# Kernel tuning notes

Measured on AMD Instinct MI355X. Metric: run time of the kernel, lower is better.

## Reference

```python
import jax, jax.numpy as jnp
import numpy as np

DIM = 1024
NB = 25            # num_basis_functions
ALPHA_X = 1.0
DT = 0.001
MAX_TIME = 10.0
TAU = 1.0
ALPHA_Y = 25.0
BETA_Y = 6.25
WEIGHT_SCALE = 1000.0
T = int(MAX_TIME / DT) + 1   # rollout buffer length = 10001


def setup_inputs() -> dict:
    key = jax.random.key(0)
    k1, k2, k3 = jax.random.split(key, 3)
    y0 = jax.random.normal(k1, (DIM,), dtype=jnp.float32)
    # learned parameters of the module
    g = jax.random.normal(k2, (DIM,), dtype=jnp.float32)
    weights = jax.random.normal(k3, (DIM, NB), dtype=jnp.float32) / NB
    return {"y0": y0, "g": g, "weights": weights}


def reference(y0, g, weights):
    # basis function centers / widths (canonical system)
    c = jnp.exp(-ALPHA_X * jnp.linspace(0.0, MAX_TIME, NB)).astype(y0.dtype)
    h = (NB / c).astype(y0.dtype)
    decay = jnp.asarray(1.0 - ALPHA_X * TAU * DT, y0.dtype)

    def step(carry, _):
        x, y, dy = carry
        x = x * decay                                   # decay_time()
        psi = jnp.exp(-h * (x - c) ** 2)                # [NB]
        # force(y0): sum over basis functions, per dim
        force = (WEIGHT_SCALE * (weights @ psi)) * x * (g - y0) / jnp.sum(psi)  # [DIM]
        ddy = ALPHA_Y * (BETA_Y * (g - y) - dy) + force
        ndy = dy + TAU * DT * ddy
        ny = y + TAU * DT * ndy
        return (x, ny, ndy), jnp.concatenate([ny, ndy])

    x0 = jnp.asarray(1.0, y0.dtype)
    dy0 = jnp.zeros_like(y0)
    _, rows = jax.lax.scan(step, (x0, y0, dy0), None, length=T - 1)  # [T-1, 2*DIM]
    first = jnp.concatenate([y0, dy0])[None]                          # [1, 2*DIM]
    ydy = jnp.concatenate([first, rows], axis=0)                      # [T, 2*DIM]
    y0rep = jnp.broadcast_to(y0, (T, DIM))
    return jnp.concatenate([y0rep, ydy], axis=1)                      # [T, 3*DIM]
```

## Files before the change

### kernel.cpp

```cpp
#include <hip/hip_runtime.h>
#include <math.h>


#define DIM    1024
#define NB     25
#define NSTEP  10000
#define CHUNKS 200
#define LSTEPS 50
#define QS     32

__global__ __launch_bounds__(64) void k_prep(float* __restrict__ q,
                                             float* __restrict__ QY,
                                             float* __restrict__ QD,
                                             double logdecay,
                                             double a00, double a01,
                                             double a10, double a11) {
    __shared__ float lq[LSTEPS][NB + 1];
    const int c = blockIdx.x;
    const int tid = threadIdx.x;
    if (tid < LSTEPS) {
        int t = c * LSTEPS + tid + 1;
        float x = (float)exp((double)t * logdecay);
        float psi[NB];
        float S = 0.f;
#pragma unroll
        for (int k = 0; k < NB; ++k) {
            float lk = (10.0f / 24.0f) * (float)k;
            float ck = expf(-lk);
            float hk = 25.0f / ck;
            float dxc = x - ck;
            float p = expf(-hk * dxc * dxc);
            psi[k] = p;
            S += p;
        }
        float scale = 1000.0f * x / S;
        float* qrow = q + (size_t)(c * LSTEPS + tid) * QS;
#pragma unroll
        for (int k = 0; k < NB; ++k) {
            float v = psi[k] * scale;
            qrow[k] = v;
            lq[tid][k] = v;
        }
    }
    __syncthreads();
    if (tid < NB) {
        double py = (double)0.001f * (double)0.001f;
        double pd = (double)0.001f;
        double qy = 0.0, qd = 0.0;
        for (int j = LSTEPS - 1; j >= 0; --j) {
            double v = (double)lq[j][tid];
            qy += py * v;
            qd += pd * v;
            double npy = a00 * py + a01 * pd;
            double npd = a10 * py + a11 * pd;
            py = npy; pd = npd;
        }
        QY[c * QS + tid] = (float)qy;
        QD[c * QS + tid] = (float)qd;
    }
}

__global__ __launch_bounds__(256) void k_dots(const float* __restrict__ QY,
                                              const float* __restrict__ QD,
                                              const float* __restrict__ W,
                                              const float* __restrict__ g,
                                              const float* __restrict__ y0,
                                              float* __restrict__ dots,
                                              double spY, double spD) {
    const int c = blockIdx.y;
    const int d = blockIdx.x * 256 + threadIdx.x;
    const float gd  = g[d];
    const float gd0 = gd - y0[d];
    float sy = 0.f, sd = 0.f;
#pragma unroll
    for (int k = 0; k < NB; ++k) {
        float wk = W[d * NB + k];
        sy += wk * QY[c * QS + k];
        sd += wk * QD[c * QS + k];
    }
    dots[c * DIM + d]                = (float)((double)gd * spY + (double)gd0 * (double)sy);
    dots[CHUNKS * DIM + c * DIM + d] = (float)((double)gd * spD + (double)gd0 * (double)sd);
}

__global__ __launch_bounds__(64) void k_scan(const float* __restrict__ dots,
                                             const float* __restrict__ y0,
                                             float* __restrict__ vs,
                                             double m00, double m01,
                                             double m10, double m11) {
    __shared__ float ls[CHUNKS][2][64];
    const int tid = threadIdx.x;
    const int d = blockIdx.x * 64 + tid;
    for (int c = 0; c < CHUNKS; ++c) {
        ls[c][0][tid] = dots[c * DIM + d];
        ls[c][1][tid] = dots[CHUNKS * DIM + c * DIM + d];
    }
    double vy = (double)y0[d], vdy = 0.0;
    for (int c = 0; c < CHUNKS; ++c) {
        vs[c * DIM + d] = (float)vy;
        vs[CHUNKS * DIM + c * DIM + d] = (float)vdy;
        double ny  = m00 * vy + m01 * vdy + (double)ls[c][0][tid];
        double ndy = m10 * vy + m11 * vdy + (double)ls[c][1][tid];
        vy = ny; vdy = ndy;
    }
}

__global__ __launch_bounds__(64) void k_roll(const float* __restrict__ q,
                                             const float* __restrict__ W,
                                             const float* __restrict__ g,
                                             const float* __restrict__ y0,
                                             const float* __restrict__ vs,
                                             float* __restrict__ out) {
    const int c = blockIdx.y;
    const int d = blockIdx.x * 64 + threadIdx.x;
    float w[NB];
#pragma unroll
    for (int k = 0; k < NB; ++k) w[k] = W[d * NB + k];
    const float y0d = y0[d];
    const float gd  = g[d];
    const float gd0 = gd - y0d;
    float y  = vs[c * DIM + d];
    float dy = vs[CHUNKS * DIM + c * DIM + d];
    if (c == 0) {
        out[d] = y0d;
        out[DIM + d] = y0d;
        out[2 * DIM + d] = 0.f;
    }
    const float* qp = q + (size_t)c * LSTEPS * QS;
    float* op = out + (size_t)(c * LSTEPS + 1) * (3 * DIM);
#pragma unroll 2
    for (int j = 0; j < LSTEPS; ++j) {
        float dot = 0.f;
#pragma unroll
        for (int k = 0; k < NB; ++k) dot += w[k] * qp[k];
        qp += QS;
        float f   = dot * gd0;
        float ddy = 25.0f * (6.25f * (gd - y) - dy) + f;
        dy = dy + 0.001f * ddy;
        y  = y + 0.001f * dy;
        op[d] = y0d;
        op[DIM + d] = y;
        op[2 * DIM + d] = dy;
        op += 3 * DIM;
    }
}

extern "C" void kernel_launch(void* const* d_in, const int* in_sizes, int n_in,
                              void* d_out, int out_size, void* d_ws, size_t ws_size,
                              hipStream_t stream) {
    const float* y0 = (const float*)d_in[0];
    const float* g  = (const float*)d_in[1];
    const float* W  = (const float*)d_in[2];
    float* out = (float*)d_out;

    float* q  = (float*)d_ws;
    float* QY = q  + (size_t)NSTEP * QS;
    float* QD = QY + (size_t)CHUNKS * QS;
    float* vs = QD + (size_t)CHUNKS * QS;
    float* dots = out;

    const double dtD = (double)0.001f;
    const double aD = 25.0, abD = 25.0 * 6.25;
    const double a00 = 1.0 - dtD * dtD * abD;
    const double a01 = dtD * (1.0 - dtD * aD);
    const double a10 = -dtD * abD;
    const double a11 = 1.0 - dtD * aD;
    double m00 = 1, m01 = 0, m10 = 0, m11 = 1;
    double py = dtD * dtD, pd = dtD, sY = 0.0, sD = 0.0;
    for (int i = 0; i < LSTEPS; ++i) {
        double t00 = a00 * m00 + a01 * m10;
        double t01 = a00 * m01 + a01 * m11;
        double t10 = a10 * m00 + a11 * m10;
        double t11 = a10 * m01 + a11 * m11;
        m00 = t00; m01 = t01; m10 = t10; m11 = t11;
        sY += py; sD += pd;
        double npy = a00 * py + a01 * pd;
        double npd = a10 * py + a11 * pd;
        py = npy; pd = npd;
    }
    const double spY = 156.25 * sY;
    const double spD = 156.25 * sD;
    const double logdecay = log((double)(1.0f - 0.001f));

    k_prep<<<CHUNKS, 64, 0, stream>>>(q, QY, QD, logdecay, a00, a01, a10, a11);
    k_dots<<<dim3(DIM / 256, CHUNKS), 256, 0, stream>>>(QY, QD, W, g, y0, dots, spY, spD);
    k_scan<<<DIM / 64, 64, 0, stream>>>(dots, y0, vs, m00, m01, m10, m11);
    k_roll<<<dim3(DIM / 64, CHUNKS), 64, 0, stream>>>(q, W, g, y0, vs, out);
}
```

Baseline: 163.5 us.

## Split chunk scan into three-level parallel scan and transpose weights for coalescing

Replaces the serial 200-chunk scan, which ran on only 16 blocks, with a three-phase scan (per-superchunk local, superchunk prefix, per-chunk fixup) run over many more threads. Adds a transpose of the weight matrix inside the prep kernel so dot and rollout kernels read weights coalesced. Stages the per-chunk psi coefficients in shared memory with float4 loads in the rollout kernel. Also changes the chunk count and length and the block sizes. This adds two extra kernel launches and more workspace traffic.

```diff
diff --git a/kernel.cpp b/kernel.cpp
--- a/kernel.cpp
+++ b/kernel.cpp
@@ -5,19 +5,29 @@
 #define DIM    1024
 #define NB     25
 #define NSTEP  10000
-#define CHUNKS 200
-#define LSTEPS 50
+#define CHUNKS 250
+#define LSTEPS 40
+#define SC     25
+#define SS     10
 #define QS     32
 
 __global__ __launch_bounds__(64) void k_prep(float* __restrict__ q,
                                              float* __restrict__ QY,
                                              float* __restrict__ QD,
+                                             float* __restrict__ WT,
+                                             const float* __restrict__ W,
                                              double logdecay,
                                              double a00, double a01,
                                              double a10, double a11) {
-    __shared__ float lq[LSTEPS][NB + 1];
     const int c = blockIdx.x;
     const int tid = threadIdx.x;
+    if (c >= CHUNKS) {
+        int k = c - CHUNKS;
+        for (int d = tid; d < DIM; d += 64)
+            WT[k * DIM + d] = W[d * NB + k];
+        return;
+    }
+    __shared__ float lq[LSTEPS][NB + 1];
     if (tid < LSTEPS) {
         int t = c * LSTEPS + tid + 1;
         float x = (float)exp((double)t * logdecay);
@@ -62,19 +72,20 @@
 
 __global__ __launch_bounds__(256) void k_dots(const float* __restrict__ QY,
                                               const float* __restrict__ QD,
-                                              const float* __restrict__ W,
+                                              const float* __restrict__ WT,
                                               const float* __restrict__ g,
                                               const float* __restrict__ y0,
                                               float* __restrict__ dots,
                                               double spY, double spD) {
-    const int c = blockIdx.y;
-    const int d = blockIdx.x * 256 + threadIdx.x;
+    const int idx = blockIdx.x * 256 + threadIdx.x;
+    const int d = idx & (DIM - 1);
+    const int c = idx >> 10;
     const float gd  = g[d];
     const float gd0 = gd - y0[d];
     float sy = 0.f, sd = 0.f;
 #pragma unroll
     for (int k = 0; k < NB; ++k) {
-        float wk = W[d * NB + k];
+        float wk = WT[k * DIM + d];
         sy += wk * QY[c * QS + k];
         sd += wk * QD[c * QS + k];
     }
@@ -82,57 +93,120 @@
     dots[CHUNKS * DIM + c * DIM + d] = (float)((double)gd * spD + (double)gd0 * (double)sd);
 }
 
-__global__ __launch_bounds__(64) void k_scan(const float* __restrict__ dots,
-                                             const float* __restrict__ y0,
-                                             float* __restrict__ vs,
-                                             double m00, double m01,
-                                             double m10, double m11) {
-    __shared__ float ls[CHUNKS][2][64];
-    const int tid = threadIdx.x;
-    const int d = blockIdx.x * 64 + tid;
-    for (int c = 0; c < CHUNKS; ++c) {
-        ls[c][0][tid] = dots[c * DIM + d];
-        ls[c][1][tid] = dots[CHUNKS * DIM + c * DIM + d];
+__global__ __launch_bounds__(256) void k_scanA(const float* __restrict__ dots,
+                                               float* __restrict__ usY,
+                                               float* __restrict__ usD,
+                                               double m00, double m01,
+                                               double m10, double m11) {
+    const int idx = blockIdx.x * 256 + threadIdx.x;
+    const int d = idx & (DIM - 1);
+    const int s = idx >> 10;
+    double vy = 0.0, vdy = 0.0;
+#pragma unroll
+    for (int i = 0; i < SS; ++i) {
+        int c = s * SS + i;
+        double ry = (double)dots[c * DIM + d];
+        double rd = (double)dots[CHUNKS * DIM + c * DIM + d];
+        double ny  = m00 * vy + m01 * vdy + ry;
+        double ndy = m10 * vy + m11 * vdy + rd;
+        vy = ny; vdy = ndy;
+    }
+    usY[s * DIM + d] = (float)vy;
+    usD[s * DIM + d] = (float)vdy;
+}
+
+__global__ __launch_bounds__(256) void k_scanB(const float* __restrict__ usY,
+                                               const float* __restrict__ usD,
+                                               const float* __restrict__ y0,
+                                               float* __restrict__ ssY,
+                                               float* __restrict__ ssD,
+                                               double b00, double b01,
+                                               double b10, double b11) {
+    const int d = blockIdx.x * 256 + threadIdx.x;
+    float uy[SC], ud[SC];
+#pragma unroll
+    for (int s = 0; s < SC; ++s) {
+        uy[s] = usY[s * DIM + d];
+        ud[s] = usD[s * DIM + d];
     }
     double vy = (double)y0[d], vdy = 0.0;
-    for (int c = 0; c < CHUNKS; ++c) {
+#pragma unroll
+    for (int s = 0; s < SC; ++s) {
+        ssY[s * DIM + d] = (float)vy;
+        ssD[s * DIM + d] = (float)vdy;
+        double ny  = b00 * vy + b01 * vdy + (double)uy[s];
+        double ndy = b10 * vy + b11 * vdy + (double)ud[s];
+        vy = ny; vdy = ndy;
+    }
+}
+
+__global__ __launch_bounds__(256) void k_scanC(const float* __restrict__ dots,
+                                               const float* __restrict__ ssY,
+                                               const float* __restrict__ ssD,
+                                               float* __restrict__ vs,
+                                               double m00, double m01,
+                                               double m10, double m11) {
+    const int idx = blockIdx.x * 256 + threadIdx.x;
+    const int d = idx & (DIM - 1);
+    const int s = idx >> 10;
+    double vy = (double)ssY[s * DIM + d];
+    double vdy = (double)ssD[s * DIM + d];
+#pragma unroll
+    for (int i = 0; i < SS; ++i) {
+        int c = s * SS + i;
         vs[c * DIM + d] = (float)vy;
         vs[CHUNKS * DIM + c * DIM + d] = (float)vdy;
-        double ny  = m00 * vy + m01 * vdy + (double)ls[c][0][tid];
-        double ndy = m10 * vy + m11 * vdy + (double)ls[c][1][tid];
+        double ry = (double)dots[c * DIM + d];
+        double rd = (double)dots[CHUNKS * DIM + c * DIM + d];
+        double ny  = m00 * vy + m01 * vdy + ry;
+        double ndy = m10 * vy + m11 * vdy + rd;
         vy = ny; vdy = ndy;
     }
 }
 
-__global__ __launch_bounds__(64) void k_roll(const float* __restrict__ q,
-                                             const float* __restrict__ W,
-                                             const float* __restrict__ g,
-                                             const float* __restrict__ y0,
-                                             const float* __restrict__ vs,
-                                             float* __restrict__ out) {
+__global__ __launch_bounds__(256) void k_roll(const float* __restrict__ q,
+                                              const float* __restrict__ WT,
+                                              const float* __restrict__ g,
+                                              const float* __restrict__ y0,
+                                              const float* __restrict__ vs,
+                                              float* __restrict__ out) {
+    __shared__ float lq[LSTEPS][QS];
     const int c = blockIdx.y;
-    const int d = blockIdx.x * 64 + threadIdx.x;
+    const int tid = threadIdx.x;
+    const int d = blockIdx.x * 256 + tid;
+    {
+        const float4* src = (const float4*)(q + (size_t)c * LSTEPS * QS);
+        float4* dst = (float4*)&lq[0][0];
+        for (int i = tid; i < LSTEPS * (QS / 4); i += 256) dst[i] = src[i];
+    }
     float w[NB];
 #pragma unroll
-    for (int k = 0; k < NB; ++k) w[k] = W[d * NB + k];
+    for (int k = 0; k < NB; ++k) w[k] = WT[k * DIM + d];
     const float y0d = y0[d];
     const float gd  = g[d];
     const float gd0 = gd - y0d;
     float y  = vs[c * DIM + d];
     float dy = vs[CHUNKS * DIM + c * DIM + d];
+    __syncthreads();
     if (c == 0) {
         out[d] = y0d;
         out[DIM + d] = y0d;
         out[2 * DIM + d] = 0.f;
     }
-    const float* qp = q + (size_t)c * LSTEPS * QS;
     float* op = out + (size_t)(c * LSTEPS + 1) * (3 * DIM);
 #pragma unroll 2
     for (int j = 0; j < LSTEPS; ++j) {
+        const float4* row = (const float4*)&lq[j][0];
         float dot = 0.f;
 #pragma unroll
-        for (int k = 0; k < NB; ++k) dot += w[k] * qp[k];
-        qp += QS;
+        for (int m = 0; m < 6; ++m) {
+            float4 qv = row[m];
+            dot += w[4 * m + 0] * qv.x;
+            dot += w[4 * m + 1] * qv.y;
+            dot += w[4 * m + 2] * qv.z;
+            dot += w[4 * m + 3] * qv.w;
+        }
+        dot += w[24] * lq[j][24];
         float f   = dot * gd0;
         float ddy = 25.0f * (6.25f * (gd - y) - dy) + f;
         dy = dy + 0.001f * ddy;
@@ -152,10 +226,15 @@
     const float* W  = (const float*)d_in[2];
     float* out = (float*)d_out;
 
-    float* q  = (float*)d_ws;
-    float* QY = q  + (size_t)NSTEP * QS;
-    float* QD = QY + (size_t)CHUNKS * QS;
-    float* vs = QD + (size_t)CHUNKS * QS;
+    float* q   = (float*)d_ws;
+    float* QY  = q   + (size_t)NSTEP * QS;
+    float* QD  = QY  + (size_t)CHUNKS * QS;
+    float* WT  = QD  + (size_t)CHUNKS * QS;
+    float* usY = WT  + (size_t)NB * DIM;
+    float* usD = usY + (size_t)SC * DIM;
+    float* ssY = usD + (size_t)SC * DIM;
+    float* ssD = ssY + (size_t)SC * DIM;
+    float* vs  = ssD + (size_t)SC * DIM;
     float* dots = out;
 
     const double dtD = (double)0.001f;
@@ -177,12 +256,22 @@
         double npd = a10 * py + a11 * pd;
         py = npy; pd = npd;
     }
+    double b00 = 1, b01 = 0, b10 = 0, b11 = 1;
+    for (int i = 0; i < SS; ++i) {
+        double t00 = m00 * b00 + m01 * b10;
+        double t01 = m00 * b01 + m01 * b11;
+        double t10 = m10 * b00 + m11 * b10;
+        double t11 = m10 * b01 + m11 * b11;
+        b00 = t00; b01 = t01; b10 = t10; b11 = t11;
+    }
     const double spY = 156.25 * sY;
     const double spD = 156.25 * sD;
     const double logdecay = log((double)(1.0f - 0.001f));
 
-    k_prep<<<CHUNKS, 64, 0, stream>>>(q, QY, QD, logdecay, a00, a01, a10, a11);
-    k_dots<<<dim3(DIM / 256, CHUNKS), 256, 0, stream>>>(QY, QD, W, g, y0, dots, spY, spD);
-    k_scan<<<DIM / 64, 64, 0, stream>>>(dots, y0, vs, m00, m01, m10, m11);
-    k_roll<<<dim3(DIM / 64, CHUNKS), 64, 0, stream>>>(q, W, g, y0, vs, out);
-}
+    k_prep<<<CHUNKS + NB, 64, 0, stream>>>(q, QY, QD, WT, W, logdecay, a00, a01, a10, a11);
+    k_dots<<<(DIM * CHUNKS) / 256, 256, 0, stream>>>(QY, QD, WT, g, y0, dots, spY, spD);
+    k_scanA<<<(DIM * SC) / 256, 256, 0, stream>>>(dots, usY, usD, m00, m01, m10, m11);
+    k_scanB<<<DIM / 256, 256, 0, stream>>>(usY, usD, y0, ssY, ssD, b00, b01, b10, b11);
+    k_scanC<<<(DIM * SC) / 256, 256, 0, stream>>>(dots, ssY, ssD, vs, m00, m01, m10, m11);
+    k_roll<<<dim3(DIM / 256, CHUNKS), 256, 0, stream>>>(q, WT, g, y0, vs, out);
+}
```

New measurement: 152.8 us. 6.5% less time.
